# Kernel tuning notes

Hardware: AMD Instinct MI355X
Metric: run time of the kernel (lower is better)

The kernel has to match this reference:

```python
import jax, jax.numpy as jnp
import numpy as np

DIM = 768
HEADS = 12
HEAD_DIM = DIM // HEADS
SCALE = HEAD_DIM ** -0.5


def setup_inputs() -> dict:
    key = jax.random.key(0)
    ks = jax.random.split(key, 6)
    B, N = 4, 2048
    x = jax.random.normal(ks[0], (B, N, DIM), dtype=jnp.float32)
    s = DIM ** -0.5
    Wq = jax.random.normal(ks[1], (DIM, DIM), dtype=jnp.float32) * s
    Wk = jax.random.normal(ks[2], (DIM, DIM), dtype=jnp.float32) * s
    Wv = jax.random.normal(ks[3], (DIM, DIM), dtype=jnp.float32) * s
    Wp = jax.random.normal(ks[4], (DIM, DIM), dtype=jnp.float32) * s
    bp = jnp.zeros((DIM,), dtype=jnp.float32)
    return {"x": x, "Wq": Wq, "Wk": Wk, "Wv": Wv, "Wp": Wp, "bp": bp}


def reference(x, Wq, Wk, Wv, Wp, bp):
    B, N, C = x.shape
    # separate Q/K/V linears (no bias, qkv_bias=False); torch Linear: x @ W.T
    q = (x @ Wq.T).reshape(B, N, HEADS, HEAD_DIM).transpose(0, 2, 1, 3)
    k = (x @ Wk.T).reshape(B, N, HEADS, HEAD_DIM).transpose(0, 2, 1, 3)
    v = (x @ Wv.T).reshape(B, N, HEADS, HEAD_DIM).transpose(0, 2, 1, 3)
    # explicit full [B,H,N,N] attention matrix, as in the source
    attn = jnp.einsum("bhqd,bhkd->bhqk", q, k) * SCALE
    attn = jax.nn.softmax(attn, axis=-1)
    out = jnp.einsum("bhqk,bhkd->bhqd", attn, v)
    out = out.transpose(0, 2, 1, 3).reshape(B, N, C)
    return out @ Wp.T + bp
```

## Files before the change

kernel.cpp:

```cpp
#include <hip/hip_runtime.h>
#include <cstdint>

#define DIM   768
#define HEADS 12
#define HDIM  64
#define BATCH 4
#define SEQ   2048
#define MROWS (BATCH*SEQ)

typedef __bf16 bf16;
typedef __bf16 bf16x4_t __attribute__((ext_vector_type(4)));
typedef __bf16 bf16x8_t __attribute__((ext_vector_type(8)));
typedef float  f32x4_t  __attribute__((ext_vector_type(4)));
typedef float  f32x16_t __attribute__((ext_vector_type(16)));

__global__ void cast_bf16_kernel(const float* __restrict__ src, bf16* __restrict__ dst, int n4) {
    int i = blockIdx.x * blockDim.x + threadIdx.x;
    if (i >= n4) return;
    const float4 v = reinterpret_cast<const float4*>(src)[i];
    bf16x4_t o;
    o[0] = (bf16)v.x; o[1] = (bf16)v.y; o[2] = (bf16)v.z; o[3] = (bf16)v.w;
    reinterpret_cast<bf16x4_t*>(dst)[i] = o;
}

__global__ void cast_w4_kernel(const float* __restrict__ s0, const float* __restrict__ s1,
                               const float* __restrict__ s2, const float* __restrict__ s3,
                               bf16* __restrict__ d0, bf16* __restrict__ d1,
                               bf16* __restrict__ d2, bf16* __restrict__ d3, int n4) {
    int i = blockIdx.x * blockDim.x + threadIdx.x;
    if (i >= n4) return;
    int y = blockIdx.y;
    const float* src = (y == 0) ? s0 : (y == 1) ? s1 : (y == 2) ? s2 : s3;
    bf16* dst        = (y == 0) ? d0 : (y == 1) ? d1 : (y == 2) ? d2 : d3;
    const float4 v = reinterpret_cast<const float4*>(src)[i];
    bf16x4_t o;
    o[0] = (bf16)v.x; o[1] = (bf16)v.y; o[2] = (bf16)v.z; o[3] = (bf16)v.w;
    reinterpret_cast<bf16x4_t*>(dst)[i] = o;
}

__device__ __forceinline__ void gload_lds16(const bf16* g, bf16* l) {
    __builtin_amdgcn_global_load_lds((const __attribute__((address_space(1))) void*)g,
                                     (__attribute__((address_space(3))) void*)l, 16, 0, 0);
}

__global__ __launch_bounds__(256, 3) void qkvv_gemm(
        const bf16* __restrict__ X,
        const bf16* __restrict__ Wq, const bf16* __restrict__ Wk, const bf16* __restrict__ Wv,
        bf16* __restrict__ Q, bf16* __restrict__ Kd, bf16* __restrict__ Vt)
{
    __shared__ __align__(16) bf16 SM[128 * 128];
    bf16* As = SM;
    bf16* Bs = SM + 128 * 64;
    const int tid  = threadIdx.x;

    const int d  = blockIdx.x + 6 * blockIdx.y + 384 * blockIdx.z;
    const int L  = (d & 7) * 144 + (d >> 3);
    const int z  = L / 384;
    const int rem = L % 384;
    const int m0 = (rem % 6) * 128;
    const int n0 = (rem / 6) * 128;

    const bf16* Ap = (z == 0) ? Wq : (z == 1 ? Wk : Wv);
    const int lane = tid & 63;
    const int w    = tid >> 6;
    const int wm   = (w & 1) * 64, wn = (w >> 1) * 64;
    const int lr   = lane & 15, quad = lane >> 4;

    f32x4_t acc[4][4] = {};

    for (int kk = 0; kk < DIM; kk += 64) {
        #pragma unroll
        for (int i = 0; i < 4; ++i) {
            int c = tid + i * 256;
            int row = c >> 3, ch = c & 7;
            int gch = ch ^ (row & 7);
            gload_lds16(Ap + (size_t)(m0 + row) * DIM + kk + gch * 8, &As[row * 64 + ch * 8]);
            gload_lds16(X  + (size_t)(n0 + row) * DIM + kk + gch * 8, &Bs[row * 64 + ch * 8]);
        }
        __syncthreads();
        #pragma unroll
        for (int ks = 0; ks < 2; ++ks) {
            bf16x8_t af[4], bfr[4];
            #pragma unroll
            for (int i = 0; i < 4; ++i) {
                int row = wm + i * 16 + lr;
                int ch = (ks * 4 + quad) ^ (row & 7);
                af[i] = *reinterpret_cast<const bf16x8_t*>(&As[row * 64 + ch * 8]);
            }
            #pragma unroll
            for (int j = 0; j < 4; ++j) {
                int row = wn + j * 16 + lr;
                int ch = (ks * 4 + quad) ^ (row & 7);
                bfr[j] = *reinterpret_cast<const bf16x8_t*>(&Bs[row * 64 + ch * 8]);
            }
            #pragma unroll
            for (int i = 0; i < 4; ++i)
                #pragma unroll
                for (int j = 0; j < 4; ++j)
                    acc[i][j] = __builtin_amdgcn_mfma_f32_16x16x32_bf16(af[i], bfr[j], acc[i][j], 0, 0, 0);
        }
        __syncthreads();
    }

    if (z == 2) {
        #pragma unroll
        for (int i = 0; i < 4; ++i) {
            int ml = wm + i * 16 + quad * 4;
            #pragma unroll
            for (int j = 0; j < 4; ++j) {
                int p   = lr >> 2;
                int pp  = ((p & 1) << 1) | (p >> 1);
                int nl  = wn + j * 16 + (pp << 2) + (lr & 3);
                #pragma unroll
                for (int r = 0; r < 4; ++r)
                    SM[(ml + r) * 128 + nl] = (bf16)acc[i][j][r];
            }
        }
        __syncthreads();
        const int rr = tid >> 4, cc = tid & 15;
        #pragma unroll
        for (int rnd = 0; rnd < 8; ++rnd) {
            int ml = rnd * 16 + rr;
            *reinterpret_cast<bf16x8_t*>(&Vt[(size_t)(m0 + ml) * MROWS + n0 + cc * 8]) =
                *reinterpret_cast<const bf16x8_t*>(&SM[ml * 128 + cc * 8]);
        }
    } else {
        const float sc = (z == 0) ? 0.18033688011112042f : 1.0f;
        bf16* dst = (z == 0) ? Q : Kd;
        #pragma unroll
        for (int i = 0; i < 4; ++i) {
            int mb = m0 + wm + i * 16 + quad * 4;
            int h  = mb >> 6, d0 = mb & 63;
            #pragma unroll
            for (int j = 0; j < 4; ++j) {
                int sample = n0 + wn + j * 16 + lr;
                int b = sample >> 11, srow = sample & 2047;
                bf16x4_t o;
                #pragma unroll
                for (int r = 0; r < 4; ++r)
                    o[r] = (bf16)(acc[i][j][r] * sc);
                *reinterpret_cast<bf16x4_t*>(
                    &dst[(((size_t)b * HEADS + h) * SEQ + srow) * HDIM + d0]) = o;
            }
        }
    }
}

__global__ __launch_bounds__(256, 4) void out_gemm(
        const bf16* __restrict__ A,
        const bf16* __restrict__ W,
        const float* __restrict__ bias,
        float* __restrict__ out)
{
    __shared__ __align__(16) bf16 As[64*64];
    __shared__ __align__(16) bf16 Bs[128*64];
    const int tid  = threadIdx.x;

    const int d  = blockIdx.x + 6 * blockIdx.y;
    const int L  = (d & 7) * 96 + (d >> 3);
    const int n0 = (L % 6) * 128;
    const int m0 = (L / 6) * 64;

    const int lane = tid & 63;
    const int w    = tid >> 6;
    const int wm   = (w & 1) * 32, wn = (w >> 1) * 64;
    const int lr   = lane & 15, quad = lane >> 4;

    f32x4_t acc[2][4] = {};

    for (int kk = 0; kk < DIM; kk += 64) {
        #pragma unroll
        for (int i = 0; i < 2; ++i) {
            int c = tid + i * 256;
            int row = c >> 3, ch = c & 7;
            int gch = ch ^ (row & 7);
            gload_lds16(A + (size_t)(m0 + row) * DIM + kk + gch * 8, &As[row * 64 + ch * 8]);
        }
        #pragma unroll
        for (int i = 0; i < 4; ++i) {
            int c = tid + i * 256;
            int row = c >> 3, ch = c & 7;
            int gch = ch ^ (row & 7);
            gload_lds16(W + (size_t)(n0 + row) * DIM + kk + gch * 8, &Bs[row * 64 + ch * 8]);
        }
        __syncthreads();
        #pragma unroll
        for (int ks = 0; ks < 2; ++ks) {
            bf16x8_t af[2], bfr[4];
            #pragma unroll
            for (int i = 0; i < 2; ++i) {
                int row = wm + i * 16 + lr;
                int ch = (ks * 4 + quad) ^ (row & 7);
                af[i] = *reinterpret_cast<const bf16x8_t*>(&As[row * 64 + ch * 8]);
            }
            #pragma unroll
            for (int j = 0; j < 4; ++j) {
                int row = wn + j * 16 + lr;
                int ch = (ks * 4 + quad) ^ (row & 7);
                bfr[j] = *reinterpret_cast<const bf16x8_t*>(&Bs[row * 64 + ch * 8]);
            }
            #pragma unroll
            for (int i = 0; i < 2; ++i)
                #pragma unroll
                for (int j = 0; j < 4; ++j)
                    acc[i][j] = __builtin_amdgcn_mfma_f32_16x16x32_bf16(af[i], bfr[j], acc[i][j], 0, 0, 0);
        }
        __syncthreads();
    }

    #pragma unroll
    for (int i = 0; i < 2; ++i) {
        int mbase = m0 + wm + i * 16 + quad * 4;
        #pragma unroll
        for (int j = 0; j < 4; ++j) {
            int n = n0 + wn + j * 16 + lr;
            float bv = bias[n];
            #pragma unroll
            for (int r = 0; r < 4; ++r) {
                int m = mbase + r;
                out[(size_t)m * DIM + n] = acc[i][j][r] + bv;
            }
        }
    }
}

__global__ __launch_bounds__(256, 3) void attn_kernel(
        const bf16* __restrict__ Q, const bf16* __restrict__ Kd,
        const bf16* __restrict__ Vt, bf16* __restrict__ Ab)
{
    __shared__ __align__(16) bf16 SH[5 * 64 * 64];
    bf16* Kb = SH;
    bf16* Vb = SH + 2 * 4096;

    const int tid  = threadIdx.x;

    const int dd = blockIdx.x + 16 * blockIdx.y;
    const int L  = (dd & 7) * 96 + (dd >> 3);
    const int bh = L >> 4;
    const int q0 = (L & 15) * 128;

    const int b    = bh / HEADS, h = bh % HEADS;
    const int lane = tid & 63, w = tid >> 6;
    const int l31  = lane & 31, hw = lane >> 5;
    const int wq   = w * 32;

    const size_t qkbase = (size_t)bh * SEQ * HDIM;
    const size_t vbase  = (size_t)h * HDIM * MROWS + (size_t)b * SEQ;

    const int src_row  = tid >> 3, src_ch = tid & 7;
    const int src_gch  = src_ch ^ (src_row & 7);
    const int src_row2 = (tid + 256) >> 3;
    const int src_gch2 = src_ch ^ (src_row2 & 7);
    const int loff1 = src_row  * 64 + src_ch * 8;
    const int loff2 = src_row2 * 64 + src_ch * 8;

    {
        bf16* Qst = Vb + 4096;
        #pragma unroll
        for (int i = 0; i < 4; ++i) {
            int c = tid + i * 256;
            int row = c >> 3, ch = c & 7;
            int gch = ch ^ (row & 7);
            gload_lds16(Q + qkbase + (size_t)(q0 + row) * HDIM + gch * 8, Qst + row * 64 + ch * 8);
        }
    }

    const bf16* kp1 = Kd + qkbase + (size_t)src_row  * HDIM + src_gch  * 8;
    const bf16* kp2 = Kd + qkbase + (size_t)src_row2 * HDIM + src_gch2 * 8;
    const bf16* vp1 = Vt + vbase  + (size_t)src_row  * MROWS + src_gch  * 8;
    const bf16* vp2 = Vt + vbase  + (size_t)src_row2 * MROWS + src_gch2 * 8;
    const ptrdiff_t kstep = 64 * HDIM, vstep = 64;

    gload_lds16(kp1, Kb + loff1); gload_lds16(kp2, Kb + loff2);
    gload_lds16(vp1, Vb + loff1); gload_lds16(vp2, Vb + loff2);
    __syncthreads();

    bf16x8_t qf[4];
    {
        const bf16* Qst = Vb + 4096;
        int row = wq + l31;
        #pragma unroll
        for (int g = 0; g < 4; ++g) {
            int ch = (2 * g + hw) ^ (row & 7);
            qf[g] = *reinterpret_cast<const bf16x8_t*>(&Qst[row * 64 + ch * 8]);
        }
    }
    __syncthreads();

    f32x16_t oacc[2] = {};
    f32x16_t rsacc  = {};
    bf16x8_t pk[4];
    bf16x8_t ones8;
    #pragma unroll
    for (int i = 0; i < 8; ++i) ones8[i] = (bf16)1.0f;

    int vprev = 2, vcur = 0, vnext = 1;

    for (int it = 0; it < SEQ / 64; ++it) {
        if (it + 1 < SEQ / 64) {
            const ptrdiff_t g = (ptrdiff_t)(it + 1);
            bf16* kd = Kb + ((it + 1) & 1) * 4096;
            bf16* vd = Vb + vnext * 4096;
            gload_lds16(kp1 + g * kstep, kd + loff1); gload_lds16(kp2 + g * kstep, kd + loff2);
            gload_lds16(vp1 + g * vstep, vd + loff1); gload_lds16(vp2 + g * vstep, vd + loff2);
        }

        const bf16* Ks = Kb + (it & 1) * 4096;

        f32x16_t sacc[2] = {};
        __builtin_amdgcn_s_setprio(1);
        #pragma unroll
        for (int kc = 0; kc < 2; ++kc) {
            int row = kc * 32 + l31;
            #pragma unroll
            for (int g = 0; g < 4; ++g) {
                int ch = (2 * g + hw) ^ (row & 7);
                bf16x8_t af = *reinterpret_cast<const bf16x8_t*>(&Ks[row * 64 + ch * 8]);
                sacc[kc] = __builtin_amdgcn_mfma_f32_32x32x16_bf16(af, qf[g], sacc[kc], 0, 0, 0);
            }
        }

        if (it > 0) {
            const bf16* Vs = Vb + vprev * 4096;
            #pragma unroll
            for (int dc = 0; dc < 2; ++dc) {
                int row = dc * 32 + l31;
                #pragma unroll
                for (int kg = 0; kg < 4; ++kg) {
                    int myc = (2 * kg + hw) ^ (row & 7);
                    bf16x8_t bb = *reinterpret_cast<const bf16x8_t*>(&Vs[row * 64 + myc * 8]);
                    oacc[dc] = __builtin_amdgcn_mfma_f32_32x32x16_bf16(pk[kg], bb, oacc[dc], 0, 0, 0);
                }
            }
            #pragma unroll
            for (int kg = 0; kg < 4; ++kg)
                rsacc = __builtin_amdgcn_mfma_f32_32x32x16_bf16(pk[kg], ones8, rsacc, 0, 0, 0);
        }
        __builtin_amdgcn_s_setprio(0);

        #pragma unroll
        for (int kg = 0; kg < 4; ++kg) {
            #pragma unroll
            for (int j = 0; j < 8; ++j)
                pk[kg][j] = (bf16)__builtin_amdgcn_exp2f(sacc[kg >> 1][(kg & 1) * 8 + j]);
        }

        __syncthreads();
        int tmp = vprev; vprev = vcur; vcur = vnext; vnext = tmp;
    }

    {
        const bf16* Vs = Vb + vprev * 4096;
        #pragma unroll
        for (int dc = 0; dc < 2; ++dc) {
            int row = dc * 32 + l31;
            #pragma unroll
            for (int kg = 0; kg < 4; ++kg) {
                int myc = (2 * kg + hw) ^ (row & 7);
                bf16x8_t bb = *reinterpret_cast<const bf16x8_t*>(&Vs[row * 64 + myc * 8]);
                oacc[dc] = __builtin_amdgcn_mfma_f32_32x32x16_bf16(pk[kg], bb, oacc[dc], 0, 0, 0);
            }
        }
        #pragma unroll
        for (int kg = 0; kg < 4; ++kg)
            rsacc = __builtin_amdgcn_mfma_f32_32x32x16_bf16(pk[kg], ones8, rsacc, 0, 0, 0);
    }

    float inv[16];
    #pragma unroll
    for (int r = 0; r < 16; ++r)
        inv[r] = 1.0f / rsacc[r];
    #pragma unroll
    for (int dc = 0; dc < 2; ++dc) {
        int d = dc * 32 + l31;
        #pragma unroll
        for (int r = 0; r < 16; ++r) {
            int q = q0 + wq + (r & 3) + 8 * (r >> 2) + 4 * hw;
            Ab[((size_t)b * SEQ + q) * DIM + h * HDIM + d] = (bf16)(oacc[dc][r] * inv[r]);
        }
    }
}

extern "C" void kernel_launch(void* const* d_in, const int* in_sizes, int n_in,
                              void* d_out, int out_size, void* d_ws, size_t ws_size,
                              hipStream_t stream) {
    (void)in_sizes; (void)n_in; (void)out_size; (void)ws_size;
    const float* x  = (const float*)d_in[0];
    const float* Wq = (const float*)d_in[1];
    const float* Wk = (const float*)d_in[2];
    const float* Wv = (const float*)d_in[3];
    const float* Wp = (const float*)d_in[4];
    const float* bp = (const float*)d_in[5];
    float* out = (float*)d_out;

    char* ws = (char*)d_ws;
    size_t off = 0;
    auto alloc = [&](size_t bytes) {
        void* p = ws + off;
        off += (bytes + 255) & ~(size_t)255;
        return p;
    };
    const size_t big = (size_t)MROWS * DIM * sizeof(bf16);
    const size_t wsz = (size_t)DIM * DIM * sizeof(bf16);
    bf16* Xb  = (bf16*)alloc(big);
    bf16* Qb  = (bf16*)alloc(big);
    bf16* Kb  = (bf16*)alloc(big);
    bf16* Vtb = (bf16*)alloc(big);
    bf16* Wqb = (bf16*)alloc(wsz);
    bf16* Wkb = (bf16*)alloc(wsz);
    bf16* Wvb = (bf16*)alloc(wsz);
    bf16* Wpb = (bf16*)alloc(wsz);
    bf16* Ab  = Xb;

    const int x4 = MROWS * DIM / 4;
    cast_bf16_kernel<<<(x4 + 255) / 256, 256, 0, stream>>>(x, Xb, x4);
    const int w4 = DIM * DIM / 4;
    cast_w4_kernel<<<dim3((w4 + 255) / 256, 4), 256, 0, stream>>>(
        Wq, Wk, Wv, Wp, Wqb, Wkb, Wvb, Wpb, w4);

    qkvv_gemm<<<dim3(DIM / 128, MROWS / 128, 3), 256, 0, stream>>>(
        Xb, Wqb, Wkb, Wvb, Qb, Kb, Vtb);

    attn_kernel<<<dim3(SEQ / 128, BATCH * HEADS), 256, 0, stream>>>(Qb, Kb, Vtb, Ab);

    out_gemm<<<dim3(DIM / 128, MROWS / 64), 256, 0, stream>>>(Ab, Wpb, bp, out);
}
```

Before: 206.2 us.

## Double-buffer LDS tiles with 32-wide K steps in projection GEMMs

```diff
diff --git a/kernel.cpp b/kernel.cpp
--- a/kernel.cpp
+++ b/kernel.cpp
@@ -43,14 +43,14 @@
                                      (__attribute__((address_space(3))) void*)l, 16, 0, 0);
 }
 
+__device__ __forceinline__ int swz4(int row) { return (row & 3) ^ ((row >> 2) & 3); }
+
 __global__ __launch_bounds__(256, 3) void qkvv_gemm(
         const bf16* __restrict__ X,
         const bf16* __restrict__ Wq, const bf16* __restrict__ Wk, const bf16* __restrict__ Wv,
         bf16* __restrict__ Q, bf16* __restrict__ Kd, bf16* __restrict__ Vt)
 {
-    __shared__ __align__(16) bf16 SM[128 * 128];
-    bf16* As = SM;
-    bf16* Bs = SM + 128 * 64;
+    __shared__ __align__(16) bf16 SM[2][2][128 * 32];
     const int tid  = threadIdx.x;
 
     const int d  = blockIdx.x + 6 * blockIdx.y + 384 * blockIdx.z;
@@ -66,43 +66,52 @@
     const int wm   = (w & 1) * 64, wn = (w >> 1) * 64;
     const int lr   = lane & 15, quad = lane >> 4;
 
+    const int sr1 = tid >> 2, sc1 = tid & 3;
+    const int sr2 = (tid + 256) >> 2;
+    const int g1 = sc1 ^ swz4(sr1);
+    const int g2 = sc1 ^ swz4(sr2);
+
     f32x4_t acc[4][4] = {};
 
-    for (int kk = 0; kk < DIM; kk += 64) {
+    {
+        gload_lds16(Ap + (size_t)(m0 + sr1) * DIM + g1 * 8, &SM[0][0][tid * 8]);
+        gload_lds16(X  + (size_t)(n0 + sr1) * DIM + g1 * 8, &SM[0][1][tid * 8]);
+        gload_lds16(Ap + (size_t)(m0 + sr2) * DIM + g2 * 8, &SM[0][0][(tid + 256) * 8]);
+        gload_lds16(X  + (size_t)(n0 + sr2) * DIM + g2 * 8, &SM[0][1][(tid + 256) * 8]);
+    }
+    __syncthreads();
+
+    int buf = 0;
+    for (int p = 0; p < DIM / 32; ++p) {
+        if (p + 1 < DIM / 32) {
+            int kk = (p + 1) * 32;
+            gload_lds16(Ap + (size_t)(m0 + sr1) * DIM + kk + g1 * 8, &SM[buf ^ 1][0][tid * 8]);
+            gload_lds16(X  + (size_t)(n0 + sr1) * DIM + kk + g1 * 8, &SM[buf ^ 1][1][tid * 8]);
+            gload_lds16(Ap + (size_t)(m0 + sr2) * DIM + kk + g2 * 8, &SM[buf ^ 1][0][(tid + 256) * 8]);
+            gload_lds16(X  + (size_t)(n0 + sr2) * DIM + kk + g2 * 8, &SM[buf ^ 1][1][(tid + 256) * 8]);
+        }
+        bf16x8_t af[4], bfr[4];
         #pragma unroll
         for (int i = 0; i < 4; ++i) {
-            int c = tid + i * 256;
-            int row = c >> 3, ch = c & 7;
-            int gch = ch ^ (row & 7);
-            gload_lds16(Ap + (size_t)(m0 + row) * DIM + kk + gch * 8, &As[row * 64 + ch * 8]);
-            gload_lds16(X  + (size_t)(n0 + row) * DIM + kk + gch * 8, &Bs[row * 64 + ch * 8]);
-        }
+            int row = wm + i * 16 + lr;
+            af[i] = *reinterpret_cast<const bf16x8_t*>(&SM[buf][0][row * 32 + (quad ^ swz4(row)) * 8]);
+        }
+        #pragma unroll
+        for (int j = 0; j < 4; ++j) {
+            int row = wn + j * 16 + lr;
+            bfr[j] = *reinterpret_cast<const bf16x8_t*>(&SM[buf][1][row * 32 + (quad ^ swz4(row)) * 8]);
+        }
+        #pragma unroll
+        for (int i = 0; i < 4; ++i)
+            #pragma unroll
+            for (int j = 0; j < 4; ++j)
+                acc[i][j] = __builtin_amdgcn_mfma_f32_16x16x32_bf16(af[i], bfr[j], acc[i][j], 0, 0, 0);
         __syncthreads();
-        #pragma unroll
-        for (int ks = 0; ks < 2; ++ks) {
-            bf16x8_t af[4], bfr[4];
-            #pragma unroll
-            for (int i = 0; i < 4; ++i) {
-                int row = wm + i * 16 + lr;
-                int ch = (ks * 4 + quad) ^ (row & 7);
-                af[i] = *reinterpret_cast<const bf16x8_t*>(&As[row * 64 + ch * 8]);
-            }
-            #pragma unroll
-            for (int j = 0; j < 4; ++j) {
-                int row = wn + j * 16 + lr;
-                int ch = (ks * 4 + quad) ^ (row & 7);
-                bfr[j] = *reinterpret_cast<const bf16x8_t*>(&Bs[row * 64 + ch * 8]);
-            }
-            #pragma unroll
-            for (int i = 0; i < 4; ++i)
-                #pragma unroll
-                for (int j = 0; j < 4; ++j)
-                    acc[i][j] = __builtin_amdgcn_mfma_f32_16x16x32_bf16(af[i], bfr[j], acc[i][j], 0, 0, 0);
-        }
-        __syncthreads();
+        buf ^= 1;
     }
 
     if (z == 2) {
+        bf16* CT = &SM[0][0][0];
         #pragma unroll
         for (int i = 0; i < 4; ++i) {
             int ml = wm + i * 16 + quad * 4;
@@ -113,7 +122,7 @@
                 int nl  = wn + j * 16 + (pp << 2) + (lr & 3);
                 #pragma unroll
                 for (int r = 0; r < 4; ++r)
-                    SM[(ml + r) * 128 + nl] = (bf16)acc[i][j][r];
+                    CT[(ml + r) * 128 + nl] = (bf16)acc[i][j][r];
             }
         }
         __syncthreads();
@@ -122,7 +131,7 @@
         for (int rnd = 0; rnd < 8; ++rnd) {
             int ml = rnd * 16 + rr;
             *reinterpret_cast<bf16x8_t*>(&Vt[(size_t)(m0 + ml) * MROWS + n0 + cc * 8]) =
-                *reinterpret_cast<const bf16x8_t*>(&SM[ml * 128 + cc * 8]);
+                *reinterpret_cast<const bf16x8_t*>(&CT[ml * 128 + cc * 8]);
         }
     } else {
         const float sc = (z == 0) ? 0.18033688011112042f : 1.0f;
@@ -152,8 +161,8 @@
         const float* __restrict__ bias,
         float* __restrict__ out)
 {
-    __shared__ __align__(16) bf16 As[64*64];
-    __shared__ __align__(16) bf16 Bs[128*64];
+    __shared__ __align__(16) bf16 SA[2][64 * 32];
+    __shared__ __align__(16) bf16 SB[2][128 * 32];
     const int tid  = threadIdx.x;
 
     const int d  = blockIdx.x + 6 * blockIdx.y;
@@ -166,46 +175,46 @@
     const int wm   = (w & 1) * 32, wn = (w >> 1) * 64;
     const int lr   = lane & 15, quad = lane >> 4;
 
+    const int sr1 = tid >> 2, sc1 = tid & 3;
+    const int sr2 = (tid + 256) >> 2;
+    const int g1 = sc1 ^ swz4(sr1);
+    const int g2 = sc1 ^ swz4(sr2);
+
     f32x4_t acc[2][4] = {};
 
-    for (int kk = 0; kk < DIM; kk += 64) {
+    {
+        gload_lds16(A + (size_t)(m0 + sr1) * DIM + g1 * 8, &SA[0][tid * 8]);
+        gload_lds16(W + (size_t)(n0 + sr1) * DIM + g1 * 8, &SB[0][tid * 8]);
+        gload_lds16(W + (size_t)(n0 + sr2) * DIM + g2 * 8, &SB[0][(tid + 256) * 8]);
+    }
+    __syncthreads();
+
+    int buf = 0;
+    for (int p = 0; p < DIM / 32; ++p) {
+        if (p + 1 < DIM / 32) {
+            int kk = (p + 1) * 32;
+            gload_lds16(A + (size_t)(m0 + sr1) * DIM + kk + g1 * 8, &SA[buf ^ 1][tid * 8]);
+            gload_lds16(W + (size_t)(n0 + sr1) * DIM + kk + g1 * 8, &SB[buf ^ 1][tid * 8]);
+            gload_lds16(W + (size_t)(n0 + sr2) * DIM + kk + g2 * 8, &SB[buf ^ 1][(tid + 256) * 8]);
+        }
+        bf16x8_t af[2], bfr[4];
         #pragma unroll
         for (int i = 0; i < 2; ++i) {
-            int c = tid + i * 256;
-            int row = c >> 3, ch = c & 7;
-            int gch = ch ^ (row & 7);
-            gload_lds16(A + (size_t)(m0 + row) * DIM + kk + gch * 8, &As[row * 64 + ch * 8]);
-        }
-        #pragma unroll
-        for (int i = 0; i < 4; ++i) {
-            int c = tid + i * 256;
-            int row = c >> 3, ch = c & 7;
-            int gch = ch ^ (row & 7);
-            gload_lds16(W + (size_t)(n0 + row) * DIM + kk + gch * 8, &Bs[row * 64 + ch * 8]);
-        }
+            int row = wm + i * 16 + lr;
+            af[i] = *reinterpret_cast<const bf16x8_t*>(&SA[buf][row * 32 + (quad ^ swz4(row)) * 8]);
+        }
+        #pragma unroll
+        for (int j = 0; j < 4; ++j) {
+            int row = wn + j * 16 + lr;
+            bfr[j] = *reinterpret_cast<const bf16x8_t*>(&SB[buf][row * 32 + (quad ^ swz4(row)) * 8]);
+        }
+        #pragma unroll
+        for (int i = 0; i < 2; ++i)
+            #pragma unroll
+            for (int j = 0; j < 4; ++j)
+                acc[i][j] = __builtin_amdgcn_mfma_f32_16x16x32_bf16(af[i], bfr[j], acc[i][j], 0, 0, 0);
         __syncthreads();
-        #pragma unroll
-        for (int ks = 0; ks < 2; ++ks) {
-            bf16x8_t af[2], bfr[4];
-            #pragma unroll
-            for (int i = 0; i < 2; ++i) {
-                int row = wm + i * 16 + lr;
-                int ch = (ks * 4 + quad) ^ (row & 7);
-                af[i] = *reinterpret_cast<const bf16x8_t*>(&As[row * 64 + ch * 8]);
-            }
-            #pragma unroll
-            for (int j = 0; j < 4; ++j) {
-                int row = wn + j * 16 + lr;
-                int ch = (ks * 4 + quad) ^ (row & 7);
-                bfr[j] = *reinterpret_cast<const bf16x8_t*>(&Bs[row * 64 + ch * 8]);
-            }
-            #pragma unroll
-            for (int i = 0; i < 2; ++i)
-                #pragma unroll
-                for (int j = 0; j < 4; ++j)
-                    acc[i][j] = __builtin_amdgcn_mfma_f32_16x16x32_bf16(af[i], bfr[j], acc[i][j], 0, 0, 0);
-        }
-        __syncthreads();
+        buf ^= 1;
     }
 
     #pragma unroll
```

Result: slower. 217.0 us (+5.3%).
